# Optimization experiments

Measured on AMD Instinct MI355X. Metric: run time of the kernel, lower is better.

Reference implementation:

```python
import jax, jax.numpy as jnp
import numpy as np

N_HEADS = 8
N_POINTS = 4
SPATIAL = np.array([[64, 64], [32, 32], [16, 16], [8, 8]], dtype=np.int32)


def setup_inputs() -> dict:
    key = jax.random.key(0)
    ks = jax.random.split(key, 12)
    d = 256
    H, L, P, N = N_HEADS, SPATIAL.shape[0], N_POINTS, 8
    lens = SPATIAL[:, 0] * SPATIAL[:, 1]
    Lin = int(lens.sum())
    Lq = Lin
    query = jax.random.normal(ks[0], (N, Lq, d), jnp.float32)
    reference_points = jax.random.uniform(ks[1], (N, Lq, L, 2), jnp.float32)
    input_flatten = jax.random.normal(ks[2], (N, Lin, d), jnp.float32)
    input_spatial_shapes = jnp.asarray(SPATIAL)
    starts = np.concatenate([[0], np.cumsum(lens)[:-1]]).astype(np.int32)
    input_level_start_index = jnp.asarray(starts)
    s = 1.0 / np.sqrt(d)
    W_off = jax.random.normal(ks[3], (H * L * P * 2, d), jnp.float32) * 0.01
    b_off = jax.random.normal(ks[4], (H * L * P * 2,), jnp.float32) * 0.5
    W_attn = jax.random.normal(ks[5], (H * L * P, d), jnp.float32) * 0.02
    b_attn = jnp.zeros((H * L * P,), jnp.float32)
    W_val = jax.random.normal(ks[6], (d, d), jnp.float32) * s
    b_val = jnp.zeros((d,), jnp.float32)
    W_out = jax.random.normal(ks[7], (d, d), jnp.float32) * s
    b_out = jnp.zeros((d,), jnp.float32)
    return {
        'query': query, 'reference_points': reference_points,
        'input_flatten': input_flatten,
        'input_spatial_shapes': input_spatial_shapes,
        'input_level_start_index': input_level_start_index,
        'W_off': W_off, 'b_off': b_off, 'W_attn': W_attn, 'b_attn': b_attn,
        'W_val': W_val, 'b_val': b_val, 'W_out': W_out, 'b_out': b_out,
    }


def _bilinear(img, Hl, Wl, x, y):
    # img: [B, Ch, Hl*Wl]; x, y: [B, Q, P] pixel coords (align_corners=False)
    # zero padding mode: out-of-range corners contribute 0
    x0 = jnp.floor(x)
    y0 = jnp.floor(y)
    wx = x - x0
    wy = y - y0

    def gather(xi, yi):
        valid = (xi >= 0) & (xi <= Wl - 1) & (yi >= 0) & (yi <= Hl - 1)
        ii = jnp.clip(xi, 0, Wl - 1).astype(jnp.int32)
        jj = jnp.clip(yi, 0, Hl - 1).astype(jnp.int32)
        idx = jj * Wl + ii  # [B, Q, P]
        B, Q, P = idx.shape
        v = jnp.take_along_axis(img, idx.reshape(B, 1, Q * P), axis=2)
        v = v.reshape(B, img.shape[1], Q, P)
        return v * valid[:, None].astype(img.dtype)

    return (gather(x0, y0) * ((1 - wx) * (1 - wy))[:, None]
            + gather(x0 + 1, y0) * (wx * (1 - wy))[:, None]
            + gather(x0, y0 + 1) * ((1 - wx) * wy)[:, None]
            + gather(x0 + 1, y0 + 1) * (wx * wy)[:, None])


def reference(query, reference_points, input_flatten, input_spatial_shapes,
              input_level_start_index, W_off, b_off, W_attn, b_attn,
              W_val, b_val, W_out, b_out):
    shapes = np.asarray(input_spatial_shapes)  # static structural metadata
    N, Lq, d = query.shape
    Lin = input_flatten.shape[1]
    L = shapes.shape[0]
    H, P = N_HEADS, N_POINTS
    Ch = d // H

    value = input_flatten @ W_val.T + b_val                       # [N, Lin, d]
    value = value.reshape(N, Lin, H, Ch).transpose(0, 2, 3, 1)    # [N, H, Ch, Lin]
    value = value.reshape(N * H, Ch, Lin)

    off = (query @ W_off.T + b_off).reshape(N, Lq, H, L, P, 2)
    attn = (query @ W_attn.T + b_attn).reshape(N, Lq, H, L * P)
    attn = jax.nn.softmax(attn, axis=-1).reshape(N, Lq, H, L, P)

    # normalizer is (W, H) per level
    norm = jnp.asarray(np.stack([shapes[:, 1], shapes[:, 0]], -1), query.dtype)
    loc = reference_points[:, :, None, :, None, :] + off / norm[None, None, None, :, None, :]

    attn_p = attn.transpose(0, 2, 1, 3, 4).reshape(N * H, Lq, L, P)
    starts = np.concatenate([[0], np.cumsum(shapes[:, 0] * shapes[:, 1])])

    out = jnp.zeros((N * H, Ch, Lq), query.dtype)
    for l in range(L):
        Hl, Wl = int(shapes[l, 0]), int(shapes[l, 1])
        v_l = value[:, :, starts[l]:starts[l + 1]]                # [B, Ch, Hl*Wl]
        g = loc[:, :, :, l].transpose(0, 2, 1, 3, 4).reshape(N * H, Lq, P, 2)
        # grid_sample align_corners=False with grid=2*loc-1 -> pixel = loc*W - 0.5
        x = g[..., 0] * Wl - 0.5
        y = g[..., 1] * Hl - 0.5
        samp = _bilinear(v_l, Hl, Wl, x, y)                       # [B, Ch, Lq, P]
        out = out + jnp.einsum('bcqp,bqp->bcq', samp, attn_p[:, :, l])

    out = out.reshape(N, H, Ch, Lq).transpose(0, 3, 1, 2).reshape(N, Lq, d)
    return out @ W_out.T + b_out
```

## Files before the change

### kernel.cpp

```cpp
#include <hip/hip_runtime.h>
#include <hip/hip_bf16.h>
#include <hip/hip_fp16.h>

#define NQ   5440
#define NB   8
#define DIM  256
#define NH   8
#define CHN  32
#define NLV  4
#define NPT  4
#define MTOT (NB * NQ)

typedef __attribute__((ext_vector_type(8))) short s16x8;
typedef __attribute__((ext_vector_type(4))) short s16x4;
typedef __attribute__((ext_vector_type(4))) float f32x4;
typedef unsigned short ushort_t;

#define WVAL 0
#define WOFF 65536
#define WATT 131072
#define WOUT 163840
#define WTOT 229376

__device__ __forceinline__ short f2bf(float x) {
    union { __hip_bfloat16 b; short s; } u;
    u.b = __float2bfloat16(x);
    return u.s;
}

__device__ __forceinline__ void gload_lds16(const void* g, void* l) {
    __builtin_amdgcn_global_load_lds(
        (const __attribute__((address_space(1))) unsigned int*)g,
        (__attribute__((address_space(3))) unsigned int*)l, 16, 0, 0);
}

__device__ __forceinline__ void cvt8b(const float* s, ushort_t* d) {
    f32x4 a = *(const f32x4*)s, b = *(const f32x4*)(s + 4);
    s16x8 v;
#pragma unroll
    for (int e = 0; e < 4; ++e) { v[e] = f2bf(a[e]); v[e + 4] = f2bf(b[e]); }
    *(s16x8*)d = v;
}

__global__ __launch_bounds__(256) void cvt_all(const float* __restrict__ inputf,
                                               const float* __restrict__ query,
                                               const float* __restrict__ wv,
                                               const float* __restrict__ wo,
                                               const float* __restrict__ wa,
                                               const float* __restrict__ wu,
                                               ushort_t* __restrict__ binf,
                                               ushort_t* __restrict__ bq,
                                               ushort_t* __restrict__ wb) {
    const int i = (blockIdx.x * 256 + threadIdx.x) * 8;
    if (blockIdx.y == 0) {
        cvt8b(inputf + i, binf + i);
    } else if (blockIdx.y == 1) {
        cvt8b(query + i, bq + i);
    } else {
        if (i >= WTOT) return;
        const float* src;
        int off;
        if (i < WOFF)      { src = wv; off = WVAL; }
        else if (i < WATT) { src = wo; off = WOFF; }
        else if (i < WOUT) { src = wa; off = WATT; }
        else               { src = wu; off = WOUT; }
        cvt8b(src + (i - off), wb + i);
    }
}

__device__ __forceinline__ void stC(float* p, float v) { *p = v; }
__device__ __forceinline__ void stC(__half* p, float v) { *p = __float2half(v); }

template <typename CT>
__device__ __forceinline__ void gemm_core(const ushort_t* __restrict__ A,
                                          const ushort_t* __restrict__ Wt,
                                          const float* __restrict__ biasT,
                                          CT* __restrict__ Ct, int ldC, int rowBase) {
    __shared__ ushort_t As[128 * 64];
    __shared__ ushort_t Ws[128 * 64];

    const int t = threadIdx.x;
    const int lane = t & 63, w = t >> 6;
    const int wm = w >> 1, wn = w & 1;
    const int lr = lane & 15, quad = lane >> 4;

    f32x4 acc[4][4];
#pragma unroll
    for (int i = 0; i < 4; ++i)
#pragma unroll
        for (int j = 0; j < 4; ++j)
#pragma unroll
            for (int r = 0; r < 4; ++r) acc[i][j][r] = 0.f;

    for (int ks = 0; ks < 4; ++ks) {
        if (ks) __syncthreads();
#pragma unroll
        for (int i = 0; i < 4; ++i) {
            const int c = t + i * 256;
            const int r = c >> 3, s = c & 7;
            const int g = (s - r) & 7;
            const int ke = ks * 64 + g * 8;
            gload_lds16(A + (size_t)(rowBase + r) * DIM + ke,
                        &As[(size_t)(i * 256 + w * 64) * 8]);
            gload_lds16(Wt + (size_t)r * DIM + ke,
                        &Ws[(size_t)(i * 256 + w * 64) * 8]);
        }
        __syncthreads();
#pragma unroll
        for (int kk = 0; kk < 64; kk += 32) {
            s16x8 afr[4], wfr[4];
            const int G = (kk >> 3) + quad;
#pragma unroll
            for (int i = 0; i < 4; ++i) {
                const int R = wm * 64 + i * 16 + lr;
                afr[i] = *(const s16x8*)&As[(R * 8 + ((G + R) & 7)) * 8];
            }
#pragma unroll
            for (int j = 0; j < 4; ++j) {
                const int R = wn * 64 + j * 16 + lr;
                wfr[j] = *(const s16x8*)&Ws[(R * 8 + ((G + R) & 7)) * 8];
            }
#pragma unroll
            for (int i = 0; i < 4; ++i)
#pragma unroll
                for (int j = 0; j < 4; ++j)
                    acc[i][j] = __builtin_amdgcn_mfma_f32_16x16x32_bf16(
                        afr[i], wfr[j], acc[i][j], 0, 0, 0);
        }
    }

    float bj[4];
#pragma unroll
    for (int j = 0; j < 4; ++j) bj[j] = biasT[wn * 64 + j * 16 + lr];
#pragma unroll
    for (int i = 0; i < 4; ++i)
#pragma unroll
        for (int r = 0; r < 4; ++r) {
            int row = rowBase + wm * 64 + i * 16 + quad * 4 + r;
#pragma unroll
            for (int j = 0; j < 4; ++j) {
                int col = wn * 64 + j * 16 + lr;
                stC(&Ct[(size_t)row * ldC + col], acc[i][j][r] + bj[j]);
            }
        }
}

__global__ __launch_bounds__(256) void gemm_fused(const ushort_t* __restrict__ binf,
                                                  const ushort_t* __restrict__ bq,
                                                  const ushort_t* __restrict__ wb,
                                                  const float* __restrict__ b_val,
                                                  const float* __restrict__ b_off,
                                                  const float* __restrict__ b_attn,
                                                  __half* __restrict__ bval,
                                                  float* __restrict__ v_off,
                                                  float* __restrict__ v_attn) {
    const int gy = blockIdx.y;
    const int rowBase = blockIdx.x * 128;
    if (gy < 2)
        gemm_core<__half>(binf, wb + WVAL + (size_t)gy * 128 * DIM,
                          b_val + gy * 128, bval + gy * 128, DIM, rowBase);
    else if (gy < 4)
        gemm_core<float>(bq, wb + WOFF + (size_t)(gy - 2) * 128 * DIM,
                         b_off + (gy - 2) * 128, v_off + (gy - 2) * 128, DIM, rowBase);
    else
        gemm_core<float>(bq, wb + WATT, b_attn, v_attn, 128, rowBase);
}

__global__ __launch_bounds__(256) void gemm_out(const ushort_t* __restrict__ A,
                                                const ushort_t* __restrict__ wb,
                                                const float* __restrict__ bias,
                                                float* __restrict__ C) {
    gemm_core<float>(A, wb + WOUT + (size_t)blockIdx.y * 128 * DIM,
                     bias + blockIdx.y * 128, C + blockIdx.y * 128, DIM,
                     blockIdx.x * 128);
}

__global__ __launch_bounds__(128) void sample_kernel(
    const float* __restrict__ refp,
    const float* __restrict__ off,
    const float* __restrict__ attn,
    const __half* __restrict__ bval,
    const int* __restrict__ shapes,
    const int* __restrict__ starts,
    ushort_t* __restrict__ sampb)
{
    const int qBase = blockIdx.x * 4;
    const int t = threadIdx.x;

    __shared__ __align__(16) int     sidx[512][4];
    __shared__ __align__(16) __half2 sww[512][4];

#pragma unroll
    for (int it = 0; it < 4; ++it) {
        const int i = t + it * 128;
        const int q4 = i >> 7, hlp = i & 127;
        const int h = hlp >> 4, lp = hlp & 15, l = lp >> 2;
        const int q = qBase + q4;
        const int n = q / NQ;
        const int Wl = shapes[2 * l + 1], Hl = shapes[2 * l];
        const float Wf = (float)Wl, Hf = (float)Hl;
        const float2 rp = *(const float2*)(refp + ((size_t)q * NLV + l) * 2);
        const float2 oo = *(const float2*)(off + (size_t)q * DIM + h * 32 + lp * 2);
        const float x = (rp.x + oo.x / Wf) * Wf - 0.5f;
        const float y = (rp.y + oo.y / Hf) * Hf - 0.5f;

        float logit = attn[(size_t)q * 128 + h * 16 + lp];
        float m = logit;
#pragma unroll
        for (int s = 8; s >= 1; s >>= 1) m = fmaxf(m, __shfl_xor(m, s, 16));
        float e = __expf(logit - m);
        float ss = e;
#pragma unroll
        for (int s = 8; s >= 1; s >>= 1) ss += __shfl_xor(ss, s, 16);
        const float aw = e / ss;

        const float xf = floorf(x), yf = floorf(y);
        const int ix = (int)xf, iy = (int)yf;
        const float wx = x - xf, wy = y - yf;
        const int ix1 = ix + 1, iy1 = iy + 1;
        const bool bx0 = (ix >= 0) & (ix < Wl);
        const bool bx1 = (ix1 >= 0) & (ix1 < Wl);
        const bool by0 = (iy >= 0) & (iy < Hl);
        const bool by1 = (iy1 >= 0) & (iy1 < Hl);
        const int cx0 = min(max(ix, 0), Wl - 1), cx1 = min(max(ix1, 0), Wl - 1);
        const int cy0 = min(max(iy, 0), Hl - 1), cy1 = min(max(iy1, 0), Hl - 1);
        const int base = n * NQ + starts[l];
        int4 id;
        id.x = (base + cy0 * Wl + cx0) << 9;
        id.y = (base + cy0 * Wl + cx1) << 9;
        id.z = (base + cy1 * Wl + cx0) << 9;
        id.w = (base + cy1 * Wl + cx1) << 9;
        __half2 wp[4];
        wp[0] = __float2half2_rn((bx0 && by0) ? aw * (1.f - wx) * (1.f - wy) : 0.f);
        wp[1] = __float2half2_rn((bx1 && by0) ? aw * wx * (1.f - wy) : 0.f);
        wp[2] = __float2half2_rn((bx0 && by1) ? aw * (1.f - wx) * wy : 0.f);
        wp[3] = __float2half2_rn((bx1 && by1) ? aw * wx * wy : 0.f);
        *(int4*)sidx[i] = id;
        *(uint4*)&sww[i][0] = *(uint4*)wp;
    }
    __syncthreads();

    const int q4 = t >> 5, r = t & 31;
    const int h = r >> 2, cg = r & 3;
    const int q = qBase + q4;
    const char* vb = (const char*)bval + h * 64 + cg * 16;

    __half2 acch[4];
    float accf[8];
#pragma unroll
    for (int e = 0; e < 4; ++e) acch[e] = __float2half2_rn(0.f);
#pragma unroll
    for (int e = 0; e < 8; ++e) accf[e] = 0.f;

#pragma unroll
    for (int j = 0; j < 16; ++j) {
        const int lp = (j + h) & 15;
        const int slot = (q4 << 7) + (h << 4) + lp;
        const int4 id = *(const int4*)sidx[slot];
        uint4 wu = *(const uint4*)&sww[slot][0];
        const __half2* wp = (const __half2*)&wu;
        int idc[4] = {id.x, id.y, id.z, id.w};
#pragma unroll
        for (int c = 0; c < 4; ++c) {
            const uint4 u = *(const uint4*)(vb + (size_t)(unsigned)idc[c]);
            const __half2* hv = (const __half2*)&u;
#pragma unroll
            for (int e = 0; e < 4; ++e) acch[e] = __hfma2(hv[e], wp[c], acch[e]);
        }
        if ((j & 3) == 3) {
#pragma unroll
            for (int e = 0; e < 4; ++e) {
                float2 f = __half22float2(acch[e]);
                accf[2 * e] += f.x;
                accf[2 * e + 1] += f.y;
                acch[e] = __float2half2_rn(0.f);
            }
        }
    }

    s16x8 o;
#pragma unroll
    for (int e = 0; e < 8; ++e) o[e] = f2bf(accf[e]);
    *(s16x8*)(sampb + (size_t)q * DIM + h * CHN + cg * 8) = o;
}

extern "C" void kernel_launch(void* const* d_in, const int* in_sizes, int n_in,
                              void* d_out, int out_size, void* d_ws, size_t ws_size,
                              hipStream_t stream) {
    const float* query  = (const float*)d_in[0];
    const float* refp   = (const float*)d_in[1];
    const float* inputf = (const float*)d_in[2];
    const int* shapes   = (const int*)d_in[3];
    const int* starts   = (const int*)d_in[4];
    const float* W_off  = (const float*)d_in[5];
    const float* b_off  = (const float*)d_in[6];
    const float* W_attn = (const float*)d_in[7];
    const float* b_attn = (const float*)d_in[8];
    const float* W_val  = (const float*)d_in[9];
    const float* b_val  = (const float*)d_in[10];
    const float* W_out  = (const float*)d_in[11];
    const float* b_out  = (const float*)d_in[12];
    float* out = (float*)d_out;

    const size_t AB = (size_t)MTOT * DIM * 2;
    char* ws = (char*)d_ws;
    ushort_t* wb    = (ushort_t*)ws;
    ushort_t* binf  = (ushort_t*)(ws + 512 * 1024);
    ushort_t* bq    = (ushort_t*)(ws + 512 * 1024 + AB);
    __half*   bval  = (__half*)(ws + 512 * 1024 + 2 * AB);
    float*    v_off = (float*)(ws + 512 * 1024 + 3 * AB);
    float*    v_attn= (float*)(ws + 512 * 1024 + 3 * AB + (size_t)MTOT * DIM * 4);
    ushort_t* sampb = binf;

    cvt_all<<<dim3(MTOT * DIM / 2048, 3), dim3(256), 0, stream>>>(
        inputf, query, W_val, W_off, W_attn, W_out, binf, bq, wb);
    gemm_fused<<<dim3(MTOT / 128, 5), dim3(256), 0, stream>>>(
        binf, bq, wb, b_val, b_off, b_attn, bval, v_off, v_attn);
    sample_kernel<<<dim3(MTOT / 4), dim3(128), 0, stream>>>(
        refp, v_off, v_attn, bval, shapes, starts, sampb);
    gemm_out<<<dim3(MTOT / 128, 2), dim3(256), 0, stream>>>(sampb, wb, b_out, out);
}
```

Baseline: 278.0 us.

## Fuse fp32-to-bf16 activation conversion into GEMM loads and store offsets/logits in fp16

```diff
diff --git a/kernel.cpp b/kernel.cpp
--- a/kernel.cpp
+++ b/kernel.cpp
@@ -12,7 +12,6 @@
 #define MTOT (NB * NQ)
 
 typedef __attribute__((ext_vector_type(8))) short s16x8;
-typedef __attribute__((ext_vector_type(4))) short s16x4;
 typedef __attribute__((ext_vector_type(4))) float f32x4;
 typedef unsigned short ushort_t;
 
@@ -42,37 +41,28 @@
     *(s16x8*)d = v;
 }
 
-__global__ __launch_bounds__(256) void cvt_all(const float* __restrict__ inputf,
-                                               const float* __restrict__ query,
-                                               const float* __restrict__ wv,
-                                               const float* __restrict__ wo,
-                                               const float* __restrict__ wa,
-                                               const float* __restrict__ wu,
-                                               ushort_t* __restrict__ binf,
-                                               ushort_t* __restrict__ bq,
-                                               ushort_t* __restrict__ wb) {
+__global__ __launch_bounds__(256) void cvt_weights(const float* __restrict__ wv,
+                                                   const float* __restrict__ wo,
+                                                   const float* __restrict__ wa,
+                                                   const float* __restrict__ wu,
+                                                   ushort_t* __restrict__ wb) {
     const int i = (blockIdx.x * 256 + threadIdx.x) * 8;
-    if (blockIdx.y == 0) {
-        cvt8b(inputf + i, binf + i);
-    } else if (blockIdx.y == 1) {
-        cvt8b(query + i, bq + i);
-    } else {
-        if (i >= WTOT) return;
-        const float* src;
-        int off;
-        if (i < WOFF)      { src = wv; off = WVAL; }
-        else if (i < WATT) { src = wo; off = WOFF; }
-        else if (i < WOUT) { src = wa; off = WATT; }
-        else               { src = wu; off = WOUT; }
-        cvt8b(src + (i - off), wb + i);
-    }
+    if (i >= WTOT) return;
+    const float* src;
+    int off;
+    if (i < WOFF)      { src = wv; off = WVAL; }
+    else if (i < WATT) { src = wo; off = WOFF; }
+    else if (i < WOUT) { src = wa; off = WATT; }
+    else               { src = wu; off = WOUT; }
+    cvt8b(src + (i - off), wb + i);
 }
 
 __device__ __forceinline__ void stC(float* p, float v) { *p = v; }
 __device__ __forceinline__ void stC(__half* p, float v) { *p = __float2half(v); }
-
-template <typename CT>
-__device__ __forceinline__ void gemm_core(const ushort_t* __restrict__ A,
+__device__ __forceinline__ void stC(ushort_t* p, float v) { *(short*)p = f2bf(v); }
+
+template <typename AT, typename CT>
+__device__ __forceinline__ void gemm_core(const AT* __restrict__ A,
                                           const ushort_t* __restrict__ Wt,
                                           const float* __restrict__ biasT,
                                           CT* __restrict__ Ct, int ldC, int rowBase) {
@@ -100,10 +90,22 @@
             const int r = c >> 3, s = c & 7;
             const int g = (s - r) & 7;
             const int ke = ks * 64 + g * 8;
-            gload_lds16(A + (size_t)(rowBase + r) * DIM + ke,
-                        &As[(size_t)(i * 256 + w * 64) * 8]);
             gload_lds16(Wt + (size_t)r * DIM + ke,
                         &Ws[(size_t)(i * 256 + w * 64) * 8]);
+            if constexpr (sizeof(AT) == 2) {
+                gload_lds16(A + (size_t)(rowBase + r) * DIM + ke,
+                            &As[(size_t)(i * 256 + w * 64) * 8]);
+            } else {
+                const float* pa = (const float*)A + (size_t)(rowBase + r) * DIM + ke;
+                f32x4 a0 = *(const f32x4*)pa, a1 = *(const f32x4*)(pa + 4);
+                s16x8 av;
+#pragma unroll
+                for (int e = 0; e < 4; ++e) {
+                    av[e] = f2bf(a0[e]);
+                    av[e + 4] = f2bf(a1[e]);
+                }
+                *(s16x8*)&As[(size_t)c * 8] = av;
+            }
         }
         __syncthreads();
 #pragma unroll
@@ -145,46 +147,48 @@
         }
 }
 
-__global__ __launch_bounds__(256) void gemm_fused(const ushort_t* __restrict__ binf,
-                                                  const ushort_t* __restrict__ bq,
+__global__ __launch_bounds__(256) void gemm_fused(const float* __restrict__ inputf,
+                                                  const float* __restrict__ query,
                                                   const ushort_t* __restrict__ wb,
                                                   const float* __restrict__ b_val,
                                                   const float* __restrict__ b_off,
                                                   const float* __restrict__ b_attn,
                                                   __half* __restrict__ bval,
-                                                  float* __restrict__ v_off,
-                                                  float* __restrict__ v_attn) {
+                                                  __half* __restrict__ v_off,
+                                                  __half* __restrict__ v_attn) {
     const int gy = blockIdx.y;
     const int rowBase = blockIdx.x * 128;
     if (gy < 2)
-        gemm_core<__half>(binf, wb + WVAL + (size_t)gy * 128 * DIM,
-                          b_val + gy * 128, bval + gy * 128, DIM, rowBase);
+        gemm_core<float, __half>(inputf, wb + WVAL + (size_t)gy * 128 * DIM,
+                                 b_val + gy * 128, bval + gy * 128, DIM, rowBase);
     else if (gy < 4)
-        gemm_core<float>(bq, wb + WOFF + (size_t)(gy - 2) * 128 * DIM,
-                         b_off + (gy - 2) * 128, v_off + (gy - 2) * 128, DIM, rowBase);
+        gemm_core<float, __half>(query, wb + WOFF + (size_t)(gy - 2) * 128 * DIM,
+                                 b_off + (gy - 2) * 128, v_off + (gy - 2) * 128, DIM,
+                                 rowBase);
     else
-        gemm_core<float>(bq, wb + WATT, b_attn, v_attn, 128, rowBase);
+        gemm_core<float, __half>(query, wb + WATT, b_attn, v_attn, 128, rowBase);
 }
 
 __global__ __launch_bounds__(256) void gemm_out(const ushort_t* __restrict__ A,
                                                 const ushort_t* __restrict__ wb,
                                                 const float* __restrict__ bias,
                                                 float* __restrict__ C) {
-    gemm_core<float>(A, wb + WOUT + (size_t)blockIdx.y * 128 * DIM,
-                     bias + blockIdx.y * 128, C + blockIdx.y * 128, DIM,
-                     blockIdx.x * 128);
+    gemm_core<ushort_t, float>(A, wb + WOUT + (size_t)blockIdx.y * 128 * DIM,
+                               bias + blockIdx.y * 128, C + blockIdx.y * 128, DIM,
+                               blockIdx.x * 128);
 }
 
 __global__ __launch_bounds__(128) void sample_kernel(
     const float* __restrict__ refp,
-    const float* __restrict__ off,
-    const float* __restrict__ attn,
+    const __half* __restrict__ off,
+    const __half* __restrict__ attn,
     const __half* __restrict__ bval,
     const int* __restrict__ shapes,
     const int* __restrict__ starts,
     ushort_t* __restrict__ sampb)
 {
-    const int qBase = blockIdx.x * 4;
+    const int n = blockIdx.x & 7;
+    const int qBase = n * NQ + (blockIdx.x >> 3) * 4;
     const int t = threadIdx.x;
 
     __shared__ __align__(16) int     sidx[512][4];
@@ -196,15 +200,15 @@
         const int q4 = i >> 7, hlp = i & 127;
         const int h = hlp >> 4, lp = hlp & 15, l = lp >> 2;
         const int q = qBase + q4;
-        const int n = q / NQ;
         const int Wl = shapes[2 * l + 1], Hl = shapes[2 * l];
         const float Wf = (float)Wl, Hf = (float)Hl;
         const float2 rp = *(const float2*)(refp + ((size_t)q * NLV + l) * 2);
-        const float2 oo = *(const float2*)(off + (size_t)q * DIM + h * 32 + lp * 2);
+        const __half2 oo2 = ((const __half2*)off)[(size_t)q * 128 + h * 16 + lp];
+        const float2 oo = __half22float2(oo2);
         const float x = (rp.x + oo.x / Wf) * Wf - 0.5f;
         const float y = (rp.y + oo.y / Hf) * Hf - 0.5f;
 
-        float logit = attn[(size_t)q * 128 + h * 16 + lp];
+        float logit = __half2float(attn[(size_t)q * 128 + h * 16 + lp]);
         float m = logit;
 #pragma unroll
         for (int s = 8; s >= 1; s >>= 1) m = fmaxf(m, __shfl_xor(m, s, 16));
@@ -304,18 +308,16 @@
 
     const size_t AB = (size_t)MTOT * DIM * 2;
     char* ws = (char*)d_ws;
-    ushort_t* wb    = (ushort_t*)ws;
-    ushort_t* binf  = (ushort_t*)(ws + 512 * 1024);
-    ushort_t* bq    = (ushort_t*)(ws + 512 * 1024 + AB);
-    __half*   bval  = (__half*)(ws + 512 * 1024 + 2 * AB);
-    float*    v_off = (float*)(ws + 512 * 1024 + 3 * AB);
-    float*    v_attn= (float*)(ws + 512 * 1024 + 3 * AB + (size_t)MTOT * DIM * 4);
-    ushort_t* sampb = binf;
-
-    cvt_all<<<dim3(MTOT * DIM / 2048, 3), dim3(256), 0, stream>>>(
-        inputf, query, W_val, W_off, W_attn, W_out, binf, bq, wb);
+    ushort_t* wb     = (ushort_t*)ws;
+    __half*   bval   = (__half*)(ws + 512 * 1024);
+    __half*   v_off  = (__half*)(ws + 512 * 1024 + AB);
+    __half*   v_attn = (__half*)(ws + 512 * 1024 + 2 * AB);
+    ushort_t* sampb  = (ushort_t*)(ws + 512 * 1024 + 2 * AB + AB / 2);
+
+    cvt_weights<<<dim3(WTOT / 2048), dim3(256), 0, stream>>>(W_val, W_off, W_attn,
+                                                             W_out, wb);
     gemm_fused<<<dim3(MTOT / 128, 5), dim3(256), 0, stream>>>(
-        binf, bq, wb, b_val, b_off, b_attn, bval, v_off, v_attn);
+        inputf, query, wb, b_val, b_off, b_attn, bval, v_off, v_attn);
     sample_kernel<<<dim3(MTOT / 4), dim3(128), 0, stream>>>(
         refp, v_off, v_attn, bval, shapes, starts, sampb);
     gemm_out<<<dim3(MTOT / 128, 2), dim3(256), 0, stream>>>(sampb, wb, b_out, out);
```

Result: faster. 257.3 us (-7.4%).
